# Performance work log

Hardware: AMD Instinct MI355X
Metric: run time of the kernel (lower is better)

Reference implementation:

```python
import jax, jax.numpy as jnp
import numpy as np

B = 262144
N_USERS = 100000
N_LOCS = 2000
N_ISBNS = 100000
SBERT_DIM = 384
NUM_CATS = 64
EMB = 48
TEMP = 0.05
ALPHA = 3.0
BETA = 1.0


def setup_inputs() -> dict:
    key = jax.random.key(0)
    ks = jax.random.split(key, 20)
    s = 0.05
    inp = {
        "user_idx": jax.random.randint(ks[0], (B,), 0, N_USERS),
        "loc_idx": jax.random.randint(ks[1], (B,), 0, N_LOCS),
        "pos_idx": jax.random.randint(ks[2], (B,), 0, N_ISBNS),
        "neg_idx": jax.random.randint(ks[3], (B,), 0, N_ISBNS),
        "user_cat_emb": jax.random.normal(ks[4], (N_USERS, EMB), jnp.float32) * s,
        "user_txt_emb": jax.random.normal(ks[5], (N_USERS, EMB), jnp.float32) * s,
        "loc_cat_emb": jax.random.normal(ks[6], (N_LOCS, EMB), jnp.float32) * s,
        "loc_txt_emb": jax.random.normal(ks[7], (N_LOCS, EMB), jnp.float32) * s,
        "sbert_matrix": jax.random.normal(ks[8], (N_ISBNS, SBERT_DIM), jnp.float32) * s,
        # multi-hot category matrix (~3 categories per book on average)
        "book_cat_mh": (jax.random.uniform(ks[9], (N_ISBNS, NUM_CATS)) < 0.05).astype(jnp.float32),
        "Wc1": jax.random.normal(ks[10], (NUM_CATS, 128), jnp.float32) * s,
        "bc1": jnp.zeros((128,), jnp.float32),
        "Wc2": jax.random.normal(ks[11], (128, EMB), jnp.float32) * s,
        "bc2": jnp.zeros((EMB,), jnp.float32),
        "Wt1": jax.random.normal(ks[12], (SBERT_DIM, 256), jnp.float32) * s,
        "bt1": jnp.zeros((256,), jnp.float32),
        "Wt2": jax.random.normal(ks[13], (256, EMB), jnp.float32) * s,
        "bt2": jnp.zeros((EMB,), jnp.float32),
    }
    return inp


def _l2norm(x):
    # tf.nn.l2_normalize: x / sqrt(max(sum(x^2), eps)), eps=1e-12
    sq = jnp.sum(x * x, axis=-1, keepdims=True)
    return x * jax.lax.rsqrt(jnp.maximum(sq, 1e-12))


def _encode_book(idx, sbert_matrix, book_cat_mh, Wc1, bc1, Wc2, bc2, Wt1, bt1, Wt2, bt2):
    b_cat_in = book_cat_mh[idx]                      # [B, NUM_CATS]
    b_txt_in = sbert_matrix[idx]                     # [B, SBERT_DIM]
    b_cat = jax.nn.relu(b_cat_in @ Wc1 + bc1) @ Wc2 + bc2   # [B, EMB]
    b_txt = jax.nn.relu(b_txt_in @ Wt1 + bt1) @ Wt2 + bt2   # [B, EMB]
    return _l2norm(ALPHA * b_cat + BETA * b_txt)


def reference(user_idx, loc_idx, pos_idx, neg_idx,
              user_cat_emb, user_txt_emb, loc_cat_emb, loc_txt_emb,
              sbert_matrix, book_cat_mh,
              Wc1, bc1, Wc2, bc2, Wt1, bt1, Wt2, bt2):
    # user tower (dropout inactive at inference)
    u = ALPHA * (user_cat_emb[user_idx] + loc_cat_emb[loc_idx]) \
        + BETA * (user_txt_emb[user_idx] + loc_txt_emb[loc_idx])
    u = _l2norm(u)
    p = _encode_book(pos_idx, sbert_matrix, book_cat_mh, Wc1, bc1, Wc2, bc2, Wt1, bt1, Wt2, bt2)
    n = _encode_book(neg_idx, sbert_matrix, book_cat_mh, Wc1, bc1, Wc2, bc2, Wt1, bt1, Wt2, bt2)
    pos_sim = jnp.sum(u * p, axis=-1) / TEMP
    neg_sim = jnp.sum(u * n, axis=-1) / TEMP
    return jnp.stack([pos_sim, neg_sim], axis=-1)  # [B, 2]
```

## Files before the change

### kernel.cpp

```cpp
#include <hip/hip_runtime.h>

#define SBD   384
#define NCATS 64
#define EMB   48
#define HT    256
#define HC    128
#define MB    64

typedef __attribute__((ext_vector_type(8))) short short8;
typedef __attribute__((ext_vector_type(4))) float f32x4;

__device__ __forceinline__ short f2bf(float x) {
    union { float f; unsigned u; } v; v.f = x;
    unsigned r = v.u + 0x7FFF + ((v.u >> 16) & 1);
    return (short)(r >> 16);
}

__device__ __forceinline__ short8 cvt8(float4 a, float4 b) {
    short8 h;
    h[0] = f2bf(a.x); h[1] = f2bf(a.y); h[2] = f2bf(a.z); h[3] = f2bf(a.w);
    h[4] = f2bf(b.x); h[5] = f2bf(b.y); h[6] = f2bf(b.z); h[7] = f2bf(b.w);
    return h;
}

__global__ void prep_weights(const float* __restrict__ Wt1, const float* __restrict__ Wt2,
                             const float* __restrict__ Wc1, const float* __restrict__ Wc2,
                             char* __restrict__ iT1, char* __restrict__ iT2,
                             char* __restrict__ iC1, char* __restrict__ iC2) {
    int t = blockIdx.x * blockDim.x + threadIdx.x;
    int stride = gridDim.x * blockDim.x;
    for (int g = t; g < 256 * 48; g += stride) {
        int n = g / 48, k0 = (g - n * 48) * 8;
        int c = k0 >> 5, kin = k0 & 31;
        short8 v;
        #pragma unroll
        for (int j = 0; j < 8; ++j) v[j] = f2bf(Wt1[(size_t)(k0 + j) * HT + n]);
        *(short8*)(iT1 + (size_t)c * 16384 + n * 64 + kin * 2) = v;
    }
    for (int g = t; g < 48 * 32; g += stride) {
        int n = g / 32, k0 = (g - n * 32) * 8;
        short8 v;
        #pragma unroll
        for (int j = 0; j < 8; ++j) v[j] = f2bf(Wt2[(size_t)(k0 + j) * EMB + n]);
        *(short8*)(iT2 + n * 512 + k0 * 2) = v;
    }
    for (int g = t; g < 128 * 8; g += stride) {
        int n = g / 8, k0 = (g - n * 8) * 8;
        short8 v;
        #pragma unroll
        for (int j = 0; j < 8; ++j) v[j] = f2bf(Wc1[(size_t)(k0 + j) * HC + n]);
        *(short8*)(iC1 + n * 128 + k0 * 2) = v;
    }
    for (int g = t; g < 48 * 16; g += stride) {
        int n = g / 16, k0 = (g - n * 16) * 8;
        short8 v;
        #pragma unroll
        for (int j = 0; j < 8; ++j) v[j] = f2bf(Wc2[(size_t)(k0 + j) * EMB + n]);
        *(short8*)(iC2 + n * 256 + k0 * 2) = v;
    }
}

__global__ __launch_bounds__(256, 2) void encode_books_mfma(
    const float* __restrict__ sbert, const float* __restrict__ mh,
    const char* __restrict__ iT1, const char* __restrict__ iT2,
    const char* __restrict__ iC1, const char* __restrict__ iC2,
    const float* __restrict__ bt1, const float* __restrict__ bt2,
    const float* __restrict__ bc1, const float* __restrict__ bc2,
    float* __restrict__ E, int nbooks)
{
    __shared__ char lds[65536];

    const int t  = threadIdx.x;
    const int w  = t >> 6;
    const int l  = t & 63;
    const int lr = l & 15;
    const int lg = l >> 4;
    const int book0 = blockIdx.x * MB;
    const int wm = w >> 1, wn = w & 1;

    const int srow = t >> 2, sk0 = (t & 3) * 8;
    const int sdst = (srow * 64 + sk0 * 2) ^ ((srow & 7) << 4);
    const size_t srb = (size_t)min(book0 + srow, nbooks - 1) * SBD + sk0;

    const char* bb1 = iT1 + wn * 8192 + lr * 64 + lg * 16;

    f32x4 acc[2][8];
    #pragma unroll
    for (int nt = 0; nt < 8; ++nt) {
        float b = bt1[wn * 128 + nt * 16 + lr];
        acc[0][nt] = (f32x4){b, b, b, b};
        acc[1][nt] = (f32x4){b, b, b, b};
    }

    float4 ar[4][2];
    short8 bb[2][8];

    #pragma unroll
    for (int c = 0; c < 3; ++c) {
        const float* p = sbert + srb + c * 32;
        ar[c][0] = *(const float4*)p;
        ar[c][1] = *(const float4*)(p + 4);
    }
    #pragma unroll
    for (int nt = 0; nt < 8; ++nt) bb[0][nt] = *(const short8*)(bb1 + nt * 1024);
    *(short8*)(lds + sdst) = cvt8(ar[0][0], ar[0][1]);
    asm volatile("s_waitcnt lgkmcnt(0)" ::: "memory");
    __builtin_amdgcn_sched_barrier(0);
    __builtin_amdgcn_s_barrier();

    const int ar0 = wm * 32 + lr, ar1 = wm * 32 + 16 + lr;
    const int aoff0 = (ar0 * 64 + lg * 16) ^ ((ar0 & 7) << 4);
    const int aoff1 = (ar1 * 64 + lg * 16) ^ ((ar1 & 7) << 4);

    #pragma unroll
    for (int c = 0; c < 12; ++c) {
        if (c + 1 < 12) {
            #pragma unroll
            for (int nt = 0; nt < 8; ++nt)
                bb[(c + 1) & 1][nt] = *(const short8*)(bb1 + (c + 1) * 16384 + nt * 1024);
        }
        if (c + 3 < 12) {
            const float* p = sbert + srb + (c + 3) * 32;
            ar[(c + 3) & 3][0] = *(const float4*)p;
            ar[(c + 3) & 3][1] = *(const float4*)(p + 4);
        }
        if (c + 1 < 12)
            *(short8*)(lds + ((c + 1) & 1) * 4096 + sdst) = cvt8(ar[(c + 1) & 3][0], ar[(c + 1) & 3][1]);
        short8 af0 = *(const short8*)(lds + (c & 1) * 4096 + aoff0);
        short8 af1 = *(const short8*)(lds + (c & 1) * 4096 + aoff1);
        #pragma unroll
        for (int nt = 0; nt < 8; ++nt) {
            acc[0][nt] = __builtin_amdgcn_mfma_f32_16x16x32_bf16(af0, bb[c & 1][nt], acc[0][nt], 0, 0, 0);
            acc[1][nt] = __builtin_amdgcn_mfma_f32_16x16x32_bf16(af1, bb[c & 1][nt], acc[1][nt], 0, 0, 0);
        }
        asm volatile("s_waitcnt lgkmcnt(0)" ::: "memory");
        __builtin_amdgcn_sched_barrier(0);
        __builtin_amdgcn_s_barrier();
    }

    #pragma unroll
    for (int mt = 0; mt < 2; ++mt)
        #pragma unroll
        for (int nt = 0; nt < 8; ++nt)
            #pragma unroll
            for (int r = 0; r < 4; ++r) {
                int row = wm * 32 + mt * 16 + lg * 4 + r;
                int col = wn * 128 + nt * 16 + lr;
                *(unsigned short*)(lds + 8192 + ((row * 512 + col * 2) ^ ((row & 7) << 4))) =
                    (unsigned short)f2bf(fmaxf(acc[mt][nt][r], 0.f));
            }
    #pragma unroll
    for (int i = 0; i < 2; ++i) {
        int g = t + 256 * i;
        int row = g >> 3, k0 = (g & 7) * 8;
        int rb = min(book0 + row, nbooks - 1);
        const float* s = mh + (size_t)rb * NCATS + k0;
        float4 v0 = *(const float4*)s, v1 = *(const float4*)(s + 4);
        *(short8*)(lds + 40960 + ((row * 128 + k0 * 2) ^ ((row & 7) << 4))) = cvt8(v0, v1);
    }
    asm volatile("s_waitcnt lgkmcnt(0)" ::: "memory");
    __builtin_amdgcn_sched_barrier(0);
    __builtin_amdgcn_s_barrier();

    const int arow = w * 16 + lr;
    const int aswz = (lr & 7) << 4;

    f32x4 acct[3];
    #pragma unroll
    for (int nt = 0; nt < 3; ++nt) { float b = bt2[nt * 16 + lr]; acct[nt] = (f32x4){b, b, b, b}; }
    #pragma unroll
    for (int ks = 0; ks < 8; ++ks) {
        short8 af = *(const short8*)(lds + 8192 + ((arow * 512 + (lg * 8 + ks * 32) * 2) ^ aswz));
        #pragma unroll
        for (int nt = 0; nt < 3; ++nt) {
            short8 bf = *(const short8*)(iT2 + (nt * 16 + lr) * 512 + (lg * 8 + ks * 32) * 2);
            acct[nt] = __builtin_amdgcn_mfma_f32_16x16x32_bf16(af, bf, acct[nt], 0, 0, 0);
        }
    }

    f32x4 accc[8];
    #pragma unroll
    for (int nt = 0; nt < 8; ++nt) { float b = bc1[nt * 16 + lr]; accc[nt] = (f32x4){b, b, b, b}; }
    #pragma unroll
    for (int ks = 0; ks < 2; ++ks) {
        short8 af = *(const short8*)(lds + 40960 + ((arow * 128 + (lg * 8 + ks * 32) * 2) ^ aswz));
        #pragma unroll
        for (int nt = 0; nt < 8; ++nt) {
            short8 bf = *(const short8*)(iC1 + (nt * 16 + lr) * 128 + (lg * 8 + ks * 32) * 2);
            accc[nt] = __builtin_amdgcn_mfma_f32_16x16x32_bf16(af, bf, accc[nt], 0, 0, 0);
        }
    }
    #pragma unroll
    for (int nt = 0; nt < 8; ++nt)
        #pragma unroll
        for (int r = 0; r < 4; ++r) {
            int row = w * 16 + lg * 4 + r, col = nt * 16 + lr;
            *(unsigned short*)(lds + 49152 + ((row * 256 + col * 2) ^ ((row & 7) << 4))) =
                (unsigned short)f2bf(fmaxf(accc[nt][r], 0.f));
        }
    asm volatile("s_waitcnt lgkmcnt(0)" ::: "memory");
    __builtin_amdgcn_sched_barrier(0);
    __builtin_amdgcn_s_barrier();

    f32x4 acc2[3];
    #pragma unroll
    for (int nt = 0; nt < 3; ++nt) { float b = bc2[nt * 16 + lr]; acc2[nt] = (f32x4){b, b, b, b}; }
    #pragma unroll
    for (int ks = 0; ks < 4; ++ks) {
        short8 af = *(const short8*)(lds + 49152 + ((arow * 256 + (lg * 8 + ks * 32) * 2) ^ aswz));
        #pragma unroll
        for (int nt = 0; nt < 3; ++nt) {
            short8 bf = *(const short8*)(iC2 + (nt * 16 + lr) * 256 + (lg * 8 + ks * 32) * 2);
            acc2[nt] = __builtin_amdgcn_mfma_f32_16x16x32_bf16(af, bf, acc2[nt], 0, 0, 0);
        }
    }

    f32x4 comb[3];
    #pragma unroll
    for (int nt = 0; nt < 3; ++nt)
        #pragma unroll
        for (int r = 0; r < 4; ++r) comb[nt][r] = 3.0f * acc2[nt][r] + acct[nt][r];
    float rn[4];
    #pragma unroll
    for (int r = 0; r < 4; ++r) {
        float ss = comb[0][r] * comb[0][r] + comb[1][r] * comb[1][r] + comb[2][r] * comb[2][r];
        ss += __shfl_xor(ss, 1); ss += __shfl_xor(ss, 2);
        ss += __shfl_xor(ss, 4); ss += __shfl_xor(ss, 8);
        rn[r] = rsqrtf(fmaxf(ss, 1e-12f));
    }
    #pragma unroll
    for (int nt = 0; nt < 3; ++nt)
        #pragma unroll
        for (int r = 0; r < 4; ++r) {
            int grow = book0 + w * 16 + lg * 4 + r;
            if (grow < nbooks) E[(size_t)grow * EMB + nt * 16 + lr] = comb[nt][r] * rn[r];
        }
}

__global__ __launch_bounds__(256) void score_kernel(
    const int* __restrict__ user_idx, const int* __restrict__ loc_idx,
    const int* __restrict__ pos_idx,  const int* __restrict__ neg_idx,
    const float* __restrict__ ucat, const float* __restrict__ utxt,
    const float* __restrict__ lcat, const float* __restrict__ ltxt,
    const float* __restrict__ E, float* __restrict__ out, int Bn)
{
    const int t    = threadIdx.x;
    const int lane = t & 15;
    const int s    = blockIdx.x * 16 + (t >> 4);
    if (s >= Bn) return;

    const int ui = user_idx[s];
    const int li = loc_idx[s];
    const int pi = pos_idx[s];
    const int ni = neg_idx[s];

    const int d0 = lane * 3;
    const float* uc = ucat + (size_t)ui * EMB + d0;
    const float* ut = utxt + (size_t)ui * EMB + d0;
    const float* lc = lcat + (size_t)li * EMB + d0;
    const float* lt = ltxt + (size_t)li * EMB + d0;
    const float* pp = E + (size_t)pi * EMB + d0;
    const float* nn = E + (size_t)ni * EMB + d0;

    float u0 = 3.0f * (uc[0] + lc[0]) + (ut[0] + lt[0]);
    float u1 = 3.0f * (uc[1] + lc[1]) + (ut[1] + lt[1]);
    float u2 = 3.0f * (uc[2] + lc[2]) + (ut[2] + lt[2]);

    float usq = u0 * u0 + u1 * u1 + u2 * u2;
    float ps  = u0 * pp[0] + u1 * pp[1] + u2 * pp[2];
    float ns  = u0 * nn[0] + u1 * nn[1] + u2 * nn[2];

    #pragma unroll
    for (int m = 1; m < 16; m <<= 1) {
        usq += __shfl_xor(usq, m);
        ps  += __shfl_xor(ps, m);
        ns  += __shfl_xor(ns, m);
    }

    if (lane == 0) {
        const float inv = rsqrtf(fmaxf(usq, 1e-12f)) * 20.0f;
        out[2 * (size_t)s + 0] = ps * inv;
        out[2 * (size_t)s + 1] = ns * inv;
    }
}

extern "C" void kernel_launch(void* const* d_in, const int* in_sizes, int n_in,
                              void* d_out, int out_size, void* d_ws, size_t ws_size,
                              hipStream_t stream) {
    const int*   user_idx = (const int*)d_in[0];
    const int*   loc_idx  = (const int*)d_in[1];
    const int*   pos_idx  = (const int*)d_in[2];
    const int*   neg_idx  = (const int*)d_in[3];
    const float* ucat     = (const float*)d_in[4];
    const float* utxt     = (const float*)d_in[5];
    const float* lcat     = (const float*)d_in[6];
    const float* ltxt     = (const float*)d_in[7];
    const float* sbert    = (const float*)d_in[8];
    const float* mh       = (const float*)d_in[9];
    const float* Wc1      = (const float*)d_in[10];
    const float* bc1      = (const float*)d_in[11];
    const float* Wc2      = (const float*)d_in[12];
    const float* bc2      = (const float*)d_in[13];
    const float* Wt1      = (const float*)d_in[14];
    const float* bt1      = (const float*)d_in[15];
    const float* Wt2      = (const float*)d_in[16];
    const float* bt2      = (const float*)d_in[17];

    const int Bn     = in_sizes[0];
    const int nbooks = in_sizes[8] / SBD;

    char* ws = (char*)d_ws;
    float* E = (float*)ws;
    size_t off = (size_t)nbooks * EMB * 4;
    off = (off + 255) & ~(size_t)255;
    char* iT1 = ws + off; off += 196608;
    char* iT2 = ws + off; off += 24576;
    char* iC1 = ws + off; off += 16384;
    char* iC2 = ws + off; off += 12288;

    hipLaunchKernelGGL(prep_weights, dim3(64), dim3(256), 0, stream,
                       Wt1, Wt2, Wc1, Wc2, iT1, iT2, iC1, iC2);

    const int nblocksA = (nbooks + MB - 1) / MB;
    hipLaunchKernelGGL(encode_books_mfma, dim3(nblocksA), dim3(256), 0, stream,
                       sbert, mh, iT1, iT2, iC1, iC2, bt1, bt2, bc1, bc2, E, nbooks);

    const int nblocksB = (Bn + 15) / 16;
    hipLaunchKernelGGL(score_kernel, dim3(nblocksB), dim3(256), 0, stream,
                       user_idx, loc_idx, pos_idx, neg_idx,
                       ucat, utxt, lcat, ltxt, E, (float*)d_out, Bn);
}
```

Measured before the change: 142.8 us.

## Stage full sbert tile in LDS upfront and drop per-chunk barriers

The kernel now loads all 12 K-chunks of the gathered sbert rows at once, converts them to bf16 and stores the whole 64x384 tile in LDS, so the first GEMM loop runs with no barriers. Multi-hot category rows are read straight into registers and converted there instead of going through LDS, and one barrier in the category-MLP path is removed because each wave only reads rows it wrote itself. LDS grows to 80 KB per block, and the upfront burst of loads raises register pressure. It also gives up overlap between loads and MFMA inside a block, relying on the second resident block to hide latency.

```diff
diff --git a/kernel.cpp b/kernel.cpp
--- a/kernel.cpp
+++ b/kernel.cpp
@@ -68,7 +68,7 @@
     const float* __restrict__ bc1, const float* __restrict__ bc2,
     float* __restrict__ E, int nbooks)
 {
-    __shared__ char lds[65536];
+    __shared__ char lds[81920];
 
     const int t  = threadIdx.x;
     const int w  = t >> 6;
@@ -79,10 +79,27 @@
     const int wm = w >> 1, wn = w & 1;
 
     const int srow = t >> 2, sk0 = (t & 3) * 8;
-    const int sdst = (srow * 64 + sk0 * 2) ^ ((srow & 7) << 4);
+    const int sswz = (srow & 7) << 4;
     const size_t srb = (size_t)min(book0 + srow, nbooks - 1) * SBD + sk0;
+    {
+        float4 ar[12][2];
+        #pragma unroll
+        for (int c = 0; c < 12; ++c) {
+            const float* p = sbert + srb + c * 32;
+            ar[c][0] = *(const float4*)p;
+            ar[c][1] = *(const float4*)(p + 4);
+        }
+        #pragma unroll
+        for (int c = 0; c < 12; ++c)
+            *(short8*)(lds + ((srow * 768 + c * 64 + sk0 * 2) ^ sswz)) = cvt8(ar[c][0], ar[c][1]);
+    }
 
     const char* bb1 = iT1 + wn * 8192 + lr * 64 + lg * 16;
+    short8 bb[2][8];
+    #pragma unroll
+    for (int nt = 0; nt < 8; ++nt) bb[0][nt] = *(const short8*)(bb1 + nt * 1024);
+
+    __syncthreads();
 
     f32x4 acc[2][8];
     #pragma unroll
@@ -91,26 +108,8 @@
         acc[0][nt] = (f32x4){b, b, b, b};
         acc[1][nt] = (f32x4){b, b, b, b};
     }
-
-    float4 ar[4][2];
-    short8 bb[2][8];
-
-    #pragma unroll
-    for (int c = 0; c < 3; ++c) {
-        const float* p = sbert + srb + c * 32;
-        ar[c][0] = *(const float4*)p;
-        ar[c][1] = *(const float4*)(p + 4);
-    }
-    #pragma unroll
-    for (int nt = 0; nt < 8; ++nt) bb[0][nt] = *(const short8*)(bb1 + nt * 1024);
-    *(short8*)(lds + sdst) = cvt8(ar[0][0], ar[0][1]);
-    asm volatile("s_waitcnt lgkmcnt(0)" ::: "memory");
-    __builtin_amdgcn_sched_barrier(0);
-    __builtin_amdgcn_s_barrier();
-
     const int ar0 = wm * 32 + lr, ar1 = wm * 32 + 16 + lr;
-    const int aoff0 = (ar0 * 64 + lg * 16) ^ ((ar0 & 7) << 4);
-    const int aoff1 = (ar1 * 64 + lg * 16) ^ ((ar1 & 7) << 4);
+    const int aswz0 = (ar0 & 7) << 4, aswz1 = (ar1 & 7) << 4;
 
     #pragma unroll
     for (int c = 0; c < 12; ++c) {
@@ -119,23 +118,13 @@
             for (int nt = 0; nt < 8; ++nt)
                 bb[(c + 1) & 1][nt] = *(const short8*)(bb1 + (c + 1) * 16384 + nt * 1024);
         }
-        if (c + 3 < 12) {
-            const float* p = sbert + srb + (c + 3) * 32;
-            ar[(c + 3) & 3][0] = *(const float4*)p;
-            ar[(c + 3) & 3][1] = *(const float4*)(p + 4);
-        }
-        if (c + 1 < 12)
-            *(short8*)(lds + ((c + 1) & 1) * 4096 + sdst) = cvt8(ar[(c + 1) & 3][0], ar[(c + 1) & 3][1]);
-        short8 af0 = *(const short8*)(lds + (c & 1) * 4096 + aoff0);
-        short8 af1 = *(const short8*)(lds + (c & 1) * 4096 + aoff1);
+        short8 af0 = *(const short8*)(lds + ((ar0 * 768 + c * 64 + lg * 16) ^ aswz0));
+        short8 af1 = *(const short8*)(lds + ((ar1 * 768 + c * 64 + lg * 16) ^ aswz1));
         #pragma unroll
         for (int nt = 0; nt < 8; ++nt) {
             acc[0][nt] = __builtin_amdgcn_mfma_f32_16x16x32_bf16(af0, bb[c & 1][nt], acc[0][nt], 0, 0, 0);
             acc[1][nt] = __builtin_amdgcn_mfma_f32_16x16x32_bf16(af1, bb[c & 1][nt], acc[1][nt], 0, 0, 0);
         }
-        asm volatile("s_waitcnt lgkmcnt(0)" ::: "memory");
-        __builtin_amdgcn_sched_barrier(0);
-        __builtin_amdgcn_s_barrier();
     }
 
     #pragma unroll
@@ -146,31 +135,31 @@
             for (int r = 0; r < 4; ++r) {
                 int row = wm * 32 + mt * 16 + lg * 4 + r;
                 int col = wn * 128 + nt * 16 + lr;
-                *(unsigned short*)(lds + 8192 + ((row * 512 + col * 2) ^ ((row & 7) << 4))) =
+                *(unsigned short*)(lds + 49152 + ((row * 512 + col * 2) ^ ((row & 7) << 4))) =
                     (unsigned short)f2bf(fmaxf(acc[mt][nt][r], 0.f));
             }
-    #pragma unroll
-    for (int i = 0; i < 2; ++i) {
-        int g = t + 256 * i;
-        int row = g >> 3, k0 = (g & 7) * 8;
-        int rb = min(book0 + row, nbooks - 1);
-        const float* s = mh + (size_t)rb * NCATS + k0;
-        float4 v0 = *(const float4*)s, v1 = *(const float4*)(s + 4);
-        *(short8*)(lds + 40960 + ((row * 128 + k0 * 2) ^ ((row & 7) << 4))) = cvt8(v0, v1);
-    }
+
+    const int arow = w * 16 + lr;
+    const size_t mrb = (size_t)min(book0 + arow, nbooks - 1) * NCATS;
+    float4 mf[2][2];
+    #pragma unroll
+    for (int ks = 0; ks < 2; ++ks) {
+        const float* p = mh + mrb + lg * 8 + ks * 32;
+        mf[ks][0] = *(const float4*)p;
+        mf[ks][1] = *(const float4*)(p + 4);
+    }
+
     asm volatile("s_waitcnt lgkmcnt(0)" ::: "memory");
     __builtin_amdgcn_sched_barrier(0);
     __builtin_amdgcn_s_barrier();
 
-    const int arow = w * 16 + lr;
     const int aswz = (lr & 7) << 4;
-
     f32x4 acct[3];
     #pragma unroll
     for (int nt = 0; nt < 3; ++nt) { float b = bt2[nt * 16 + lr]; acct[nt] = (f32x4){b, b, b, b}; }
     #pragma unroll
     for (int ks = 0; ks < 8; ++ks) {
-        short8 af = *(const short8*)(lds + 8192 + ((arow * 512 + (lg * 8 + ks * 32) * 2) ^ aswz));
+        short8 af = *(const short8*)(lds + 49152 + ((arow * 512 + (lg * 8 + ks * 32) * 2) ^ aswz));
         #pragma unroll
         for (int nt = 0; nt < 3; ++nt) {
             short8 bf = *(const short8*)(iT2 + (nt * 16 + lr) * 512 + (lg * 8 + ks * 32) * 2);
@@ -183,31 +172,31 @@
     for (int nt = 0; nt < 8; ++nt) { float b = bc1[nt * 16 + lr]; accc[nt] = (f32x4){b, b, b, b}; }
     #pragma unroll
     for (int ks = 0; ks < 2; ++ks) {
-        short8 af = *(const short8*)(lds + 40960 + ((arow * 128 + (lg * 8 + ks * 32) * 2) ^ aswz));
+        short8 af = cvt8(mf[ks][0], mf[ks][1]);
         #pragma unroll
         for (int nt = 0; nt < 8; ++nt) {
             short8 bf = *(const short8*)(iC1 + (nt * 16 + lr) * 128 + (lg * 8 + ks * 32) * 2);
             accc[nt] = __builtin_amdgcn_mfma_f32_16x16x32_bf16(af, bf, accc[nt], 0, 0, 0);
         }
     }
+
     #pragma unroll
     for (int nt = 0; nt < 8; ++nt)
         #pragma unroll
         for (int r = 0; r < 4; ++r) {
             int row = w * 16 + lg * 4 + r, col = nt * 16 + lr;
-            *(unsigned short*)(lds + 49152 + ((row * 256 + col * 2) ^ ((row & 7) << 4))) =
+            *(unsigned short*)(lds + ((row * 256 + col * 2) ^ ((row & 7) << 4))) =
                 (unsigned short)f2bf(fmaxf(accc[nt][r], 0.f));
         }
     asm volatile("s_waitcnt lgkmcnt(0)" ::: "memory");
     __builtin_amdgcn_sched_barrier(0);
-    __builtin_amdgcn_s_barrier();
 
     f32x4 acc2[3];
     #pragma unroll
     for (int nt = 0; nt < 3; ++nt) { float b = bc2[nt * 16 + lr]; acc2[nt] = (f32x4){b, b, b, b}; }
     #pragma unroll
     for (int ks = 0; ks < 4; ++ks) {
-        short8 af = *(const short8*)(lds + 49152 + ((arow * 256 + (lg * 8 + ks * 32) * 2) ^ aswz));
+        short8 af = *(const short8*)(lds + ((arow * 256 + (lg * 8 + ks * 32) * 2) ^ aswz));
         #pragma unroll
         for (int nt = 0; nt < 3; ++nt) {
             short8 bf = *(const short8*)(iC2 + (nt * 16 + lr) * 256 + (lg * 8 + ks * 32) * 2);
```

Measured after the change: 174.1 us. +21.9%, slower.
